# Kernel optimization log

Measured on AMD Instinct MI355X. Metric: run time of the kernel, lower is better.

The kernel has to match this reference:

```python
import jax, jax.numpy as jnp
import numpy as np

N, K, D = 65536, 1024, 256


def setup_inputs() -> dict:
    key = jax.random.key(0)
    k1, k2 = jax.random.split(key)
    e = jax.random.normal(k1, (N, D), dtype=jnp.float32)
    # module inits codebook uniform in [-1/K, 1/K]
    weight = jax.random.uniform(k2, (K, D), dtype=jnp.float32,
                                minval=-1.0 / K, maxval=1.0 / K)
    return {"e": e, "weight": weight}


def reference(e, weight):
    distances = (jnp.sum(e * e, axis=1, keepdims=True)
                 - 2.0 * jnp.matmul(e, weight.T)
                 + jnp.sum(weight * weight, axis=1))
    encoding_indices = jnp.argmin(distances, axis=1)            # [N]
    # one-hot @ weight is just a gather
    quantized = weight[encoding_indices]                        # [N, D]
    commitment_loss = jnp.mean((jax.lax.stop_gradient(quantized) - e) ** 2)
    counts = jnp.zeros((K,), dtype=jnp.float32).at[encoding_indices].add(1.0)
    codebook_usage = counts.max() / counts.sum()
    # straight-through estimator
    quantized = e + jax.lax.stop_gradient(quantized - e)
    return quantized, encoding_indices, commitment_loss, codebook_usage
```

## Files before the change

kernel.cpp:

```cpp
#include <hip/hip_runtime.h>

typedef __attribute__((ext_vector_type(8))) short short8;
typedef __attribute__((ext_vector_type(4))) float floatx4;

#define N_ROWS 65536
#define K_CB   1024
#define D_DIM  256

#define TAU 3.0e-4f
#define BLINE 520

#define OFF_RN     0
#define OFF_WN     262144
#define OFF_FIXCNT 266240
#define OFF_HIST   266496
#define OFF_IDX    270592
#define OFF_LIST   532736
#define OFF_PART   794880
#define OFF_WFRAG  827392
#define OFF_KEYS   1351680
#define OFF_WT     1875968

__device__ __forceinline__ float pw128_sq(const float4* p) {
#pragma clang fp contract(off)
    float4 q0 = p[0], q1 = p[1];
    float r0 = q0.x * q0.x, r1 = q0.y * q0.y, r2 = q0.z * q0.z, r3 = q0.w * q0.w;
    float r4 = q1.x * q1.x, r5 = q1.y * q1.y, r6 = q1.z * q1.z, r7 = q1.w * q1.w;
    for (int i = 1; i < 16; ++i) {
        float4 u0 = p[2 * i], u1 = p[2 * i + 1];
        r0 = r0 + u0.x * u0.x; r1 = r1 + u0.y * u0.y;
        r2 = r2 + u0.z * u0.z; r3 = r3 + u0.w * u0.w;
        r4 = r4 + u1.x * u1.x; r5 = r5 + u1.y * u1.y;
        r6 = r6 + u1.z * u1.z; r7 = r7 + u1.w * u1.w;
    }
    return ((r0 + r1) + (r2 + r3)) + ((r4 + r5) + (r6 + r7));
}
__device__ __forceinline__ float rownorm_np(const float* row) {
#pragma clang fp contract(off)
    float s0 = pw128_sq((const float4*)row);
    float s1 = pw128_sq((const float4*)(row + 128));
    return s0 + s1;
}
__device__ __forceinline__ float np_dist(float A, float m, float Ck) {
#pragma clang fp contract(off)
    float Bv = 2.0f * m;
    float t  = A - Bv;
    return t + Ck;
}
__device__ __forceinline__ unsigned short bf16_rne(float x) {
    unsigned u = __float_as_uint(x);
    unsigned r = u + 0x7fff + ((u >> 16) & 1);
    return (unsigned short)(r >> 16);
}
__device__ __forceinline__ float bf16_tof(unsigned short h) {
    return __uint_as_float(((unsigned)h) << 16);
}

#define PRS 260
__global__ __launch_bounds__(256) void k_prep(
        const float* __restrict__ eg, const float* __restrict__ wg,
        float* __restrict__ rn, float* __restrict__ wn,
        unsigned short* __restrict__ wfrag, float* __restrict__ wt) {
    __shared__ __align__(16) float es[32 * PRS];
    const int tid = threadIdx.x;
    const int bx  = blockIdx.x;
    if (bx < 2048) {
        const int rowBase = bx * 32;
        #pragma unroll
        for (int j = 0; j < 8; ++j) {
            int f4 = j * 256 + tid;
            int row = f4 >> 6, k4 = f4 & 63;
            float4 v = *(const float4*)(eg + (size_t)(rowBase + row) * D_DIM + k4 * 4);
            *(float4*)&es[row * PRS + k4 * 4] = v;
        }
        __syncthreads();
        if (tid < 64) {
            int row = tid >> 1, half = tid & 1;
            float s = pw128_sq((const float4*)&es[row * PRS + half * 128]);
            float so = __shfl_xor(s, 1, 64);
            if (half == 0) rn[rowBase + row] = s + so;
        }
    } else if (bx < 2052) {
        int row = (bx - 2048) * 256 + tid;
        wn[row] = rownorm_np(wg + (size_t)row * D_DIM);
    } else if (bx < 2180) {
        int t = (bx - 2052) * 256 + tid;
        int col = t >> 5, kc = t & 31;
        const float4* src = (const float4*)(wg + (size_t)col * D_DIM + kc * 8);
        float4 v0 = src[0], v1 = src[1];
        const float a[8] = {v0.x, v0.y, v0.z, v0.w, v1.x, v1.y, v1.z, v1.w};
        short8 h;
        #pragma unroll
        for (int i = 0; i < 8; ++i) h[i] = (short)bf16_rne(a[i]);
        *(short8*)(wfrag + ((size_t)kc * 1024 + col) * 8) = h;
    } else {
        float (*tw)[PRS] = (float(*)[PRS])es;
        const int cb = bx - 2180;
        const int c0 = cb * 32;
        #pragma unroll
        for (int it = 0; it < 8; ++it) {
            int idx = it * 256 + tid;
            int code = idx >> 6, f4 = idx & 63;
            *(float4*)&tw[code][f4 * 4] =
                *(const float4*)(wg + (size_t)(c0 + code) * D_DIM + f4 * 4);
        }
        __syncthreads();
        const int j = tid & 31, dg = tid >> 5;
        #pragma unroll
        for (int dd = 0; dd < 32; ++dd) {
            int d = dd * 8 + dg;
            wt[(size_t)d * K_CB + c0 + j] = tw[j][d];
        }
    }
}

__global__ __launch_bounds__(256, 4) void k_dist(
        const float* __restrict__ eg, const unsigned short* __restrict__ wfrag,
        const float* __restrict__ wn,
        int* __restrict__ idx_ws, int* __restrict__ fixlist, int* __restrict__ fixcnt) {
    __shared__ __align__(16) unsigned short Bs[32 * BLINE];
    __shared__ float wnS[K_CB];
    const int tid  = threadIdx.x;
    const int lane = tid & 63;
    const int wv   = tid >> 6;
    const int q    = lane >> 4;
    const int m15  = lane & 15;
    const int waveRow = blockIdx.x * 64 + wv * 16;

    #pragma unroll
    for (int i = 0; i < 4; ++i) wnS[tid + i * 256] = wn[tid + i * 256];

    short8 afh[8], afl[8];
    {
        const float* rowp = eg + (size_t)(waveRow + m15) * D_DIM + q * 8;
        #pragma unroll
        for (int win = 0; win < 8; ++win) {
            const float4* pa = (const float4*)(rowp + win * 32);
            float4 x0 = pa[0], x1 = pa[1];
            const float a[8] = {x0.x, x0.y, x0.z, x0.w, x1.x, x1.y, x1.z, x1.w};
            short8 h, l;
            #pragma unroll
            for (int i = 0; i < 8; ++i) {
                unsigned short hh = bf16_rne(a[i]);
                h[i] = (short)hh;
                l[i] = (short)bf16_rne(a[i] - bf16_tof(hh));
            }
            afh[win] = h;
            afl[win] = l;
        }
    }

    float best[4], sec[4];
    int bidx[4];
    #pragma unroll
    for (int s = 0; s < 4; ++s) { best[s] = 3.4e38f; sec[s] = 3.4e38f; bidx[s] = 0; }

    for (int cb = 0; cb < 16; ++cb) {
        __syncthreads();
        #pragma unroll
        for (int t = 0; t < 8; ++t) {
            int L = wv * 8 + t;
            const unsigned short* src = wfrag + ((size_t)L * 1024 + cb * 64) * 8 + lane * 8;
            __builtin_amdgcn_global_load_lds(
                (const __attribute__((address_space(1))) unsigned int*)src,
                (__attribute__((address_space(3))) unsigned int*)&Bs[L * BLINE],
                16, 0, 0);
        }
        __syncthreads();

        floatx4 acc[4];
        #pragma unroll
        for (int nt = 0; nt < 4; ++nt)
            acc[nt] = (floatx4){0.f, 0.f, 0.f, 0.f};

        #pragma unroll
        for (int nt = 0; nt < 4; ++nt) {
            #pragma unroll
            for (int win = 0; win < 8; ++win) {
                int kc = win * 4 + q;
                short8 bfh = *(short8*)&Bs[kc * BLINE + (nt * 16 + m15) * 8];
                acc[nt] = __builtin_amdgcn_mfma_f32_16x16x32_bf16(afh[win], bfh, acc[nt], 0, 0, 0);
                acc[nt] = __builtin_amdgcn_mfma_f32_16x16x32_bf16(afl[win], bfh, acc[nt], 0, 0, 0);
            }
        }
        #pragma unroll
        for (int nt = 0; nt < 4; ++nt) {
            int col = cb * 64 + nt * 16 + m15;
            float Ck = wnS[col];
            #pragma unroll
            for (int reg = 0; reg < 4; ++reg) {
                float d = __builtin_fmaf(-2.0f, acc[nt][reg], Ck);
                bool lt = d < best[reg];
                sec[reg]  = __builtin_amdgcn_fmed3f(d, best[reg], sec[reg]);
                best[reg] = fminf(d, best[reg]);
                bidx[reg] = lt ? col : bidx[reg];
            }
        }
    }

    #pragma unroll
    for (int s = 0; s < 4; ++s) {
        float b = best[s], se = sec[s];
        int ix = bidx[s];
        #pragma unroll
        for (int m = 1; m < 16; m <<= 1) {
            float bo = __shfl_xor(b, m, 64);
            float so = __shfl_xor(se, m, 64);
            int   io = __shfl_xor(ix, m, 64);
            float ns = fminf(fminf(se, so), fmaxf(b, bo));
            if (bo < b || (bo == b && io < ix)) { b = bo; ix = io; }
            se = ns;
        }
        if (m15 == 0) {
            int row = waveRow + q * 4 + s;
            idx_ws[row] = ix;
            if (se - b < TAU) {
                int p = atomicAdd(fixcnt, 1);
                fixlist[p] = row;
            }
        }
    }
}

#define FG_ROWS 8
__global__ __launch_bounds__(256) void k_fixup(
        const float* __restrict__ eg, const float* __restrict__ wt,
        const float* __restrict__ rn, const float* __restrict__ wnorm,
        const int* __restrict__ fixlist, const int* __restrict__ fixcnt,
        unsigned long long* __restrict__ keys) {
    __shared__ double xs[FG_ROWS][D_DIM];
    const int tid = threadIdx.x;
    const int cnt = *fixcnt;
    if (cnt == 0) return;
    const int ngroups = (cnt + FG_ROWS - 1) / FG_ROWS;
    const int ntiles  = ngroups * 2;
    const int rowg = tid >> 7;
    const int cg   = tid & 127;
    for (int t = blockIdx.x; t < ntiles; t += gridDim.x) {
        const int g     = t >> 1;
        const int chunk = t & 1;
        __syncthreads();
        int rows[FG_ROWS];
        #pragma unroll
        for (int i = 0; i < FG_ROWS; ++i) {
            int j = g * FG_ROWS + i;
            rows[i] = fixlist[j < cnt ? j : cnt - 1];
        }
        #pragma unroll
        for (int i = 0; i < FG_ROWS; ++i)
            xs[i][tid] = (double)eg[(size_t)rows[i] * D_DIM + tid];
        __syncthreads();

        const int c0 = chunk * 512 + cg * 4;
        float An[4];
        #pragma unroll
        for (int r = 0; r < 4; ++r) An[r] = rn[rows[rowg * 4 + r]];
        float Cw[4];
        #pragma unroll
        for (int c = 0; c < 4; ++c) Cw[c] = wnorm[c0 + c];

        double s[4][4];
        #pragma unroll
        for (int r = 0; r < 4; ++r)
            #pragma unroll
            for (int c = 0; c < 4; ++c) s[r][c] = 0.0;

        #pragma unroll 2
        for (int d = 0; d < D_DIM; d += 2) {
            float4 wa = *(const float4*)(wt + (size_t)d * K_CB + c0);
            float4 wb = *(const float4*)(wt + (size_t)(d + 1) * K_CB + c0);
            double wad[4] = {(double)wa.x, (double)wa.y, (double)wa.z, (double)wa.w};
            double wbd[4] = {(double)wb.x, (double)wb.y, (double)wb.z, (double)wb.w};
            #pragma unroll
            for (int r = 0; r < 4; ++r) {
                double2 e2 = *(const double2*)&xs[rowg * 4 + r][d];
                #pragma unroll
                for (int c = 0; c < 4; ++c)
                    s[r][c] += e2.x * wad[c] + e2.y * wbd[c];
            }
        }

        #pragma unroll
        for (int r = 0; r < 4; ++r) {
            unsigned long long key = 0xFFFFFFFFFFFFFFFFull;
            #pragma unroll
            for (int c = 0; c < 4; ++c) {
                float dq = np_dist(An[r], (float)s[r][c], Cw[c]);
                unsigned u = __float_as_uint(dq);
                unsigned key32 = u ^ (((unsigned)((int)u >> 31)) | 0x80000000u);
                unsigned long long kk =
                    ((unsigned long long)key32 << 32) | (unsigned)(c0 + c);
                key = kk < key ? kk : key;
            }
            #pragma unroll
            for (int m = 1; m < 64; m <<= 1) {
                unsigned long long o = __shfl_xor(key, m, 64);
                key = (o < key) ? o : key;
            }
            int j = g * FG_ROWS + rowg * 4 + r;
            if ((tid & 63) == 0 && j < cnt) atomicMin(&keys[j], key);
        }
    }
}

__global__ void k_fixscatter(const int* __restrict__ fixlist, const int* __restrict__ fixcnt,
                             const unsigned long long* __restrict__ keys,
                             int* __restrict__ idx_ws) {
    const int cnt = *fixcnt;
    for (int j = blockIdx.x * blockDim.x + threadIdx.x; j < cnt;
         j += gridDim.x * blockDim.x)
        idx_ws[fixlist[j]] = (int)(keys[j] & 0xFFFFFFFFull);
}

__global__ void k_final(const float* __restrict__ eg, const float* __restrict__ wg,
                        const int* __restrict__ idx_ws, float* __restrict__ qout,
                        float* __restrict__ iout, int* __restrict__ hist,
                        double* __restrict__ partials) {
    const int tid  = threadIdx.x;
    const int sub  = tid >> 6;
    const int lane = tid & 63;
    const int rowBase = blockIdx.x * 16;
    double acc = 0.0;
    #pragma unroll
    for (int g = 0; g < 4; ++g) {
        int row = rowBase + g * 4 + sub;
        int k = idx_ws[row];
        float4 ev = ((const float4*)(eg + (size_t)row * D_DIM))[lane];
        float4 wv = ((const float4*)(wg + (size_t)k   * D_DIM))[lane];
        float dx = wv.x - ev.x, dy = wv.y - ev.y, dz = wv.z - ev.z, dw = wv.w - ev.w;
        float4 qv = {ev.x + dx, ev.y + dy, ev.z + dz, ev.w + dw};
        ((float4*)(qout + (size_t)row * D_DIM))[lane] = qv;
        acc += (double)(dx * dx) + (double)(dy * dy)
             + (double)(dz * dz) + (double)(dw * dw);
        if (lane == 0) {
            iout[row] = (float)k;
            atomicAdd(&hist[k], 1);
        }
    }
    __shared__ double red[256];
    red[tid] = acc;
    __syncthreads();
    for (int st = 128; st > 0; st >>= 1) {
        if (tid < st) red[tid] += red[tid + st];
        __syncthreads();
    }
    if (tid == 0) partials[blockIdx.x] = red[0];
}

__global__ void k_scalars(const int* __restrict__ hist, const double* __restrict__ partials,
                          float* __restrict__ sout) {
    const int tid = threadIdx.x;
    double s = 0.0;
    for (int j = tid; j < N_ROWS / 16; j += 256) s += partials[j];
    int m = 0;
    for (int j = tid; j < K_CB; j += 256) m = max(m, hist[j]);
    __shared__ double rs[256];
    __shared__ int    rm[256];
    rs[tid] = s; rm[tid] = m;
    __syncthreads();
    for (int st = 128; st > 0; st >>= 1) {
        if (tid < st) { rs[tid] += rs[tid + st]; rm[tid] = max(rm[tid], rm[tid + st]); }
        __syncthreads();
    }
    if (tid == 0) {
        sout[0] = (float)(rs[0] / (double)((size_t)N_ROWS * D_DIM));
        sout[1] = (float)rm[0] / 65536.0f;
    }
}

extern "C" void kernel_launch(void* const* d_in, const int* in_sizes, int n_in,
                              void* d_out, int out_size, void* d_ws, size_t ws_size,
                              hipStream_t stream) {
    const float* e = (const float*)d_in[0];
    const float* w = (const float*)d_in[1];
    float* out  = (float*)d_out;
    float* qout = out;
    float* iout = out + (size_t)N_ROWS * D_DIM;
    float* sout = iout + N_ROWS;

    char* ws = (char*)d_ws;
    float*  rn       = (float*) (ws + OFF_RN);
    float*  wn       = (float*) (ws + OFF_WN);
    int*    fixcnt   = (int*)   (ws + OFF_FIXCNT);
    int*    hist     = (int*)   (ws + OFF_HIST);
    int*    idxp     = (int*)   (ws + OFF_IDX);
    int*    list     = (int*)   (ws + OFF_LIST);
    double* partials = (double*)(ws + OFF_PART);
    unsigned short* wfrag = (unsigned short*)(ws + OFF_WFRAG);
    unsigned long long* keys = (unsigned long long*)(ws + OFF_KEYS);
    float*  wt       = (float*) (ws + OFF_WT);

    hipMemsetAsync(ws + OFF_FIXCNT, 0, 4352, stream);
    hipMemsetAsync(ws + OFF_KEYS, 0xFF, 524288, stream);

    hipLaunchKernelGGL(k_prep,       dim3(2212),        dim3(256), 0, stream, e, w, rn, wn, wfrag, wt);
    hipLaunchKernelGGL(k_dist,       dim3(1024),        dim3(256), 0, stream, e, wfrag, wn, idxp, list, fixcnt);
    hipLaunchKernelGGL(k_fixup,      dim3(2048),        dim3(256), 0, stream, e, wt, rn, wn, list, fixcnt, keys);
    hipLaunchKernelGGL(k_fixscatter, dim3(64),          dim3(256), 0, stream, list, fixcnt, keys, idxp);
    hipLaunchKernelGGL(k_final,      dim3(N_ROWS / 16), dim3(256), 0, stream, e, w, idxp, qout, iout, hist, partials);
    hipLaunchKernelGGL(k_scalars,    dim3(1),           dim3(256), 0, stream, hist, partials, sout);
}
```

Measured before the change: 347.1 us.

## Compute row norms lazily in fixup instead of a full prep pass

Drops the k_prep pass that read all 65536 input rows to compute their squared norms. The fixup kernel now computes the norm only for the rows it rechecks, from the double copies already staged in shared memory, and adds a barrier before the values are read. This removes a full 64 MB read of the input from the prep stage. The k_dist launch bound also drops from 4 to 2 waves-per-SIMD minimum, which gives the compiler more registers but may lower occupancy.

```diff
diff --git a/kernel.cpp b/kernel.cpp
--- a/kernel.cpp
+++ b/kernel.cpp
@@ -10,7 +10,6 @@
 #define TAU 3.0e-4f
 #define BLINE 520
 
-#define OFF_RN     0
 #define OFF_WN     262144
 #define OFF_FIXCNT 266240
 #define OFF_HIST   266496
@@ -35,6 +34,17 @@
     }
     return ((r0 + r1) + (r2 + r3)) + ((r4 + r5) + (r6 + r7));
 }
+__device__ __forceinline__ float pw128_sq_lds(const double* p) {
+#pragma clang fp contract(off)
+    float r[8];
+    #pragma unroll
+    for (int j = 0; j < 8; ++j) { float x = (float)p[j]; r[j] = x * x; }
+    for (int i = 1; i < 16; ++i) {
+        #pragma unroll
+        for (int j = 0; j < 8; ++j) { float x = (float)p[8 * i + j]; r[j] = r[j] + x * x; }
+    }
+    return ((r[0] + r[1]) + (r[2] + r[3])) + ((r[4] + r[5]) + (r[6] + r[7]));
+}
 __device__ __forceinline__ float rownorm_np(const float* row) {
 #pragma clang fp contract(off)
     float s0 = pw128_sq((const float4*)row);
@@ -58,33 +68,17 @@
 
 #define PRS 260
 __global__ __launch_bounds__(256) void k_prep(
-        const float* __restrict__ eg, const float* __restrict__ wg,
-        float* __restrict__ rn, float* __restrict__ wn,
+        const float* __restrict__ wg,
+        float* __restrict__ wn,
         unsigned short* __restrict__ wfrag, float* __restrict__ wt) {
     __shared__ __align__(16) float es[32 * PRS];
     const int tid = threadIdx.x;
     const int bx  = blockIdx.x;
-    if (bx < 2048) {
-        const int rowBase = bx * 32;
-        #pragma unroll
-        for (int j = 0; j < 8; ++j) {
-            int f4 = j * 256 + tid;
-            int row = f4 >> 6, k4 = f4 & 63;
-            float4 v = *(const float4*)(eg + (size_t)(rowBase + row) * D_DIM + k4 * 4);
-            *(float4*)&es[row * PRS + k4 * 4] = v;
-        }
-        __syncthreads();
-        if (tid < 64) {
-            int row = tid >> 1, half = tid & 1;
-            float s = pw128_sq((const float4*)&es[row * PRS + half * 128]);
-            float so = __shfl_xor(s, 1, 64);
-            if (half == 0) rn[rowBase + row] = s + so;
-        }
-    } else if (bx < 2052) {
-        int row = (bx - 2048) * 256 + tid;
+    if (bx < 4) {
+        int row = bx * 256 + tid;
         wn[row] = rownorm_np(wg + (size_t)row * D_DIM);
-    } else if (bx < 2180) {
-        int t = (bx - 2052) * 256 + tid;
+    } else if (bx < 132) {
+        int t = (bx - 4) * 256 + tid;
         int col = t >> 5, kc = t & 31;
         const float4* src = (const float4*)(wg + (size_t)col * D_DIM + kc * 8);
         float4 v0 = src[0], v1 = src[1];
@@ -95,7 +89,7 @@
         *(short8*)(wfrag + ((size_t)kc * 1024 + col) * 8) = h;
     } else {
         float (*tw)[PRS] = (float(*)[PRS])es;
-        const int cb = bx - 2180;
+        const int cb = bx - 132;
         const int c0 = cb * 32;
         #pragma unroll
         for (int it = 0; it < 8; ++it) {
@@ -114,7 +108,7 @@
     }
 }
 
-__global__ __launch_bounds__(256, 4) void k_dist(
+__global__ __launch_bounds__(256, 2) void k_dist(
         const float* __restrict__ eg, const unsigned short* __restrict__ wfrag,
         const float* __restrict__ wn,
         int* __restrict__ idx_ws, int* __restrict__ fixlist, int* __restrict__ fixcnt) {
@@ -225,10 +219,11 @@
 #define FG_ROWS 8
 __global__ __launch_bounds__(256) void k_fixup(
         const float* __restrict__ eg, const float* __restrict__ wt,
-        const float* __restrict__ rn, const float* __restrict__ wnorm,
+        const float* __restrict__ wnorm,
         const int* __restrict__ fixlist, const int* __restrict__ fixcnt,
         unsigned long long* __restrict__ keys) {
     __shared__ double xs[FG_ROWS][D_DIM];
+    __shared__ float AnS[FG_ROWS];
     const int tid = threadIdx.x;
     const int cnt = *fixcnt;
     if (cnt == 0) return;
@@ -251,10 +246,14 @@
             xs[i][tid] = (double)eg[(size_t)rows[i] * D_DIM + tid];
         __syncthreads();
 
+        if (tid < 16) {
+            int row = tid >> 1, half = tid & 1;
+            float s = pw128_sq_lds(&xs[row][half * 128]);
+            float so = __shfl_xor(s, 1, 64);
+            if (half == 0) AnS[row] = s + so;
+        }
+
         const int c0 = chunk * 512 + cg * 4;
-        float An[4];
-        #pragma unroll
-        for (int r = 0; r < 4; ++r) An[r] = rn[rows[rowg * 4 + r]];
         float Cw[4];
         #pragma unroll
         for (int c = 0; c < 4; ++c) Cw[c] = wnorm[c0 + c];
@@ -279,13 +278,15 @@
                     s[r][c] += e2.x * wad[c] + e2.y * wbd[c];
             }
         }
+        __syncthreads();
 
         #pragma unroll
         for (int r = 0; r < 4; ++r) {
+            float An = AnS[rowg * 4 + r];
             unsigned long long key = 0xFFFFFFFFFFFFFFFFull;
             #pragma unroll
             for (int c = 0; c < 4; ++c) {
-                float dq = np_dist(An[r], (float)s[r][c], Cw[c]);
+                float dq = np_dist(An, (float)s[r][c], Cw[c]);
                 unsigned u = __float_as_uint(dq);
                 unsigned key32 = u ^ (((unsigned)((int)u >> 31)) | 0x80000000u);
                 unsigned long long kk =
@@ -379,7 +380,6 @@
     float* sout = iout + N_ROWS;
 
     char* ws = (char*)d_ws;
-    float*  rn       = (float*) (ws + OFF_RN);
     float*  wn       = (float*) (ws + OFF_WN);
     int*    fixcnt   = (int*)   (ws + OFF_FIXCNT);
     int*    hist     = (int*)   (ws + OFF_HIST);
@@ -393,9 +393,9 @@
     hipMemsetAsync(ws + OFF_FIXCNT, 0, 4352, stream);
     hipMemsetAsync(ws + OFF_KEYS, 0xFF, 524288, stream);
 
-    hipLaunchKernelGGL(k_prep,       dim3(2212),        dim3(256), 0, stream, e, w, rn, wn, wfrag, wt);
+    hipLaunchKernelGGL(k_prep,       dim3(164),         dim3(256), 0, stream, w, wn, wfrag, wt);
     hipLaunchKernelGGL(k_dist,       dim3(1024),        dim3(256), 0, stream, e, wfrag, wn, idxp, list, fixcnt);
-    hipLaunchKernelGGL(k_fixup,      dim3(2048),        dim3(256), 0, stream, e, wt, rn, wn, list, fixcnt, keys);
+    hipLaunchKernelGGL(k_fixup,      dim3(2048),        dim3(256), 0, stream, e, wt, wn, list, fixcnt, keys);
     hipLaunchKernelGGL(k_fixscatter, dim3(64),          dim3(256), 0, stream, list, fixcnt, keys, idxp);
     hipLaunchKernelGGL(k_final,      dim3(N_ROWS / 16), dim3(256), 0, stream, e, w, idxp, qout, iout, hist, partials);
     hipLaunchKernelGGL(k_scalars,    dim3(1),           dim3(256), 0, stream, hist, partials, sout);
```

Result: faster. 315.1 us (-9.2%).
